# Performance work log

Measured on AMD Instinct MI355X. Metric: run time of the kernel, lower is better.

Reference implementation:

```python
import jax, jax.numpy as jnp
import numpy as np

N_NODES = 20000
N_EDGES = 160000
F_IN = 512
HIDDEN = 512
N_CLASSES = 40


def setup_inputs() -> dict:
    key = jax.random.key(0)
    k1, k2, k3, k4 = jax.random.split(key, 4)
    x = jax.random.normal(k1, (N_NODES, F_IN), dtype=jnp.float32)
    edge_index = jax.random.randint(k2, (2, N_EDGES), 0, N_NODES, dtype=jnp.int64)
    # Glorot-ish init scale for the linear weights
    W1 = jax.random.normal(k3, (F_IN, HIDDEN), dtype=jnp.float32) / np.sqrt(F_IN)
    b1 = jnp.zeros((HIDDEN,), dtype=jnp.float32)
    W2 = jax.random.normal(k4, (HIDDEN, N_CLASSES), dtype=jnp.float32) / np.sqrt(HIDDEN)
    b2 = jnp.zeros((N_CLASSES,), dtype=jnp.float32)
    return {"x": x, "edge_index": edge_index, "W1": W1, "b1": b1, "W2": W2, "b2": b2}


def _gcn_conv(x, W, b, src, dst, n_nodes):
    """PyG GCNConv: h = D^-1/2 (A+I) D^-1/2 (x W) + b, self-loops already in src/dst."""
    h = x @ W  # [N, out]
    deg = jax.ops.segment_sum(jnp.ones_like(dst, dtype=h.dtype), dst, num_segments=n_nodes)
    deg_inv_sqrt = jnp.where(deg > 0, jax.lax.rsqrt(jnp.maximum(deg, 1.0)), 0.0)
    norm = deg_inv_sqrt[src] * deg_inv_sqrt[dst]  # [E]
    msg = h[src] * norm[:, None]  # [E, out]
    return jax.ops.segment_sum(msg, dst, num_segments=n_nodes) + b


def reference(x, edge_index, W1, b1, W2, b2):
    n = x.shape[0]
    loop = jnp.arange(n, dtype=edge_index.dtype)
    src = jnp.concatenate([edge_index[0], loop])  # add self-loops
    dst = jnp.concatenate([edge_index[1], loop])
    h = _gcn_conv(x, W1, b1, src, dst, n)
    h = jax.nn.relu(h)
    # dropout(p=0.5) is identity in eval mode
    out = _gcn_conv(h, W2, b2, src, dst, n)
    return out
```

## Files before the change

kernel.cpp:

```cpp
#include <hip/hip_runtime.h>
#include <hip/hip_bf16.h>
#include <stdint.h>

#define N_NODES  20000
#define N_EDGES  160000
#define N_CLS    40
#define M_PAD    20096
#define CNT_PAD  20480
#define CAP      64

typedef __bf16 bf16;
typedef __attribute__((ext_vector_type(8))) __bf16 bf16x8;
typedef __attribute__((ext_vector_type(4))) float floatx4;

__device__ inline floatx4 zero4() { floatx4 z = {0.f, 0.f, 0.f, 0.f}; return z; }

typedef __attribute__((address_space(3))) uint32_t lds_u32;
typedef __attribute__((address_space(1))) const uint32_t glb_u32;
__device__ inline void ldst16(const void* g, void* l) {
    __builtin_amdgcn_global_load_lds((glb_u32*)g, (lds_u32*)l, 16, 0, 0);
}

struct Params {
    const float* x; const int* ei; const float* W1; const float* b1;
    const float* W2; const float* b2; float* out;
    bf16 *w1t, *w2p, *h1; float* h2;
    int *cnt, *colb;
};

#define S0_ZERO 20
#define S0_W1T  128
#define S0_W2P  96
#define S0_TOT  (S0_ZERO + S0_W1T + S0_W2P)
#define NB_G1   640
#define NB_FILL 625

__global__ __launch_bounds__(256) void k_s0(Params p) {
    const int vb = blockIdx.x, tid = threadIdx.x;
    if (vb < S0_ZERO) {
        int4* dz = (int4*)(p.cnt) + vb * 256 + tid;
        *dz = make_int4(0, 0, 0, 0);
    } else if (vb < S0_ZERO + S0_W1T) {
        int t  = (vb - S0_ZERO) * 256 + tid;
        int n  = t & 511;
        int k0 = (t >> 9) * 8;
        bf16x8 v;
        for (int j = 0; j < 8; ++j) v[j] = (bf16)p.W1[((k0 + j) << 9) + n];
        *(bf16x8*)(p.w1t + n * 512 + k0) = v;
    } else {
        int t = (vb - S0_ZERO - S0_W1T) * 256 + tid;
        int j = t & 7; int e = t >> 3;
        int lane = e & 63; e >>= 6;
        int nb = e % 3; int kt = e / 3;
        int k = kt * 32 + (lane >> 4) * 8 + j;
        int n = nb * 16 + (lane & 15);
        float v = (n < N_CLS) ? p.W2[k * N_CLS + n] : 0.f;
        p.w2p[t] = (bf16)v;
    }
}

__global__ __launch_bounds__(256) void k_g1f(Params p) {
    if (blockIdx.x >= NB_G1) {
        int e = (blockIdx.x - NB_G1) * 256 + threadIdx.x;
        if (e < N_EDGES) {
            int d = p.ei[N_EDGES + e];
            int j = atomicAdd(&p.cnt[d], 1);
            if (j < CAP) p.colb[d * CAP + j] = p.ei[e];
        }
        return;
    }
    const int g  = blockIdx.x;
    const int mi = (g >> 5) * 8 + (g & 7);
    const int ni = (g >> 3) & 3;
    if (mi >= 157) return;
    __shared__ float Asf[2][128 * 32];
    __shared__ bf16  Bs[2][128 * 32];
    const int tid  = threadIdx.x;
    const int lane = tid & 63;
    const int w    = tid >> 6;
    const int wm   = w >> 1, wn = w & 1;
    const int m0   = mi * 128;
    const int n0   = ni * 128;
    const int fr   = lane & 15, fq = lane >> 4;

    floatx4 acc[4][4];
    for (int mb = 0; mb < 4; ++mb)
        for (int nb = 0; nb < 4; ++nb) acc[mb][nb] = zero4();

    const int sr  = lane >> 2;
    const int skB = (((lane & 3) ^ ((lane >> 3) & 3))) * 8;
    const bf16* Bg = p.w1t + (long)(n0 + w * 32 + sr) * 512 + skB;

    const int arl = lane >> 3;
    const int ac  = (lane & 7) ^ arl;
    const float* Agp[4];
    for (int q = 0; q < 4; ++q) {
        int gr = m0 + w * 32 + q * 8 + arl;
        if (gr > N_NODES - 1) gr = N_NODES - 1;
        Agp[q] = p.x + (long)gr * 512 + ac * 4;
    }
    const int wofA = w * 1024;
    const int wofB = w * 1024;

    for (int q = 0; q < 4; ++q)
        ldst16(Agp[q], Asf[0] + wofA + q * 256);
    ldst16(Bg,            Bs[0] + wofB);
    ldst16(Bg + 16 * 512, Bs[0] + wofB + 512);

    const int fqsB = (fq ^ ((fr >> 1) & 3)) * 8;
    const int sA0  = (((fq << 1)    ) ^ (fr & 7)) * 4;
    const int sA1  = (((fq << 1) | 1) ^ (fr & 7)) * 4;

    for (int kt = 0; kt < 16; ++kt) {
        const int cur = kt & 1, nxt = cur ^ 1;
        __syncthreads();
        if (kt < 15) {
            const int k1 = (kt + 1) * 32;
            for (int q = 0; q < 4; ++q)
                ldst16(Agp[q] + k1, Asf[nxt] + wofA + q * 256);
            ldst16(Bg + k1,            Bs[nxt] + wofB);
            ldst16(Bg + k1 + 16 * 512, Bs[nxt] + wofB + 512);
        }
        bf16x8 af[4], bfv[4];
        for (int mb = 0; mb < 4; ++mb) {
            const float* rp = Asf[cur] + (wm * 64 + mb * 16 + fr) * 32;
            float4 lo = *(const float4*)(rp + sA0);
            float4 hi = *(const float4*)(rp + sA1);
            bf16x8 v;
            v[0] = (bf16)lo.x; v[1] = (bf16)lo.y; v[2] = (bf16)lo.z; v[3] = (bf16)lo.w;
            v[4] = (bf16)hi.x; v[5] = (bf16)hi.y; v[6] = (bf16)hi.z; v[7] = (bf16)hi.w;
            af[mb] = v;
        }
        for (int nb = 0; nb < 4; ++nb)
            bfv[nb] = *(const bf16x8*)(Bs[cur] + (wn * 64 + nb * 16 + fr) * 32 + fqsB);
        for (int mb = 0; mb < 4; ++mb)
            for (int nb = 0; nb < 4; ++nb)
                acc[mb][nb] = __builtin_amdgcn_mfma_f32_16x16x32_bf16(af[mb], bfv[nb], acc[mb][nb], 0, 0, 0);
    }
    for (int mb = 0; mb < 4; ++mb)
        for (int nb = 0; nb < 4; ++nb) {
            int row0 = m0 + wm * 64 + mb * 16 + fq * 4;
            int c    = n0 + wn * 64 + nb * 16 + fr;
            for (int r = 0; r < 4; ++r)
                p.h1[(long)(row0 + r) * 512 + c] = (bf16)acc[mb][nb][r];
        }
}

__global__ __launch_bounds__(256) void k_agg1g2(Params p) {
    __shared__ bf16 t[16 * 512];
    const int tid = threadIdx.x, l = tid & 63, w = tid >> 6;
    const int ib = blockIdx.x * 16;

    const float4* bp = (const float4*)(p.b1 + l * 8);
    float4 c0 = bp[0], c1 = bp[1];
    float bb[8] = {c0.x, c0.y, c0.z, c0.w, c1.x, c1.y, c1.z, c1.w};

    for (int q4 = 0; q4 < 4; ++q4) {
        const int r = w * 4 + q4;
        const int i = ib + r;
        bf16x8 o;
        if (i >= N_NODES) {
            for (int j = 0; j < 8; ++j) o[j] = (bf16)0.f;
        } else {
            const int ci = p.cnt[i];
            const float di = rsqrtf((float)(ci + 1));
            float acc[8];
            {
                bf16x8 v = *(const bf16x8*)(p.h1 + (long)i * 512 + l * 8);
                const float wi = di * di;
                for (int j = 0; j < 8; ++j) acc[j] = (float)v[j] * wi;
            }
            const int e1 = ci < CAP ? ci : CAP;
            const int* rowcol = p.colb + (long)i * CAP;
            int e = 0;
            for (; e + 8 <= e1; e += 8) {
                int4 sa = *(const int4*)(rowcol + e);
                int4 sb = *(const int4*)(rowcol + e + 4);
                float wgt[8];
                wgt[0] = rsqrtf((float)(p.cnt[sa.x] + 1)) * di;
                wgt[1] = rsqrtf((float)(p.cnt[sa.y] + 1)) * di;
                wgt[2] = rsqrtf((float)(p.cnt[sa.z] + 1)) * di;
                wgt[3] = rsqrtf((float)(p.cnt[sa.w] + 1)) * di;
                wgt[4] = rsqrtf((float)(p.cnt[sb.x] + 1)) * di;
                wgt[5] = rsqrtf((float)(p.cnt[sb.y] + 1)) * di;
                wgt[6] = rsqrtf((float)(p.cnt[sb.z] + 1)) * di;
                wgt[7] = rsqrtf((float)(p.cnt[sb.w] + 1)) * di;
                bf16x8 u[8];
                u[0] = *(const bf16x8*)(p.h1 + (long)sa.x * 512 + l * 8);
                u[1] = *(const bf16x8*)(p.h1 + (long)sa.y * 512 + l * 8);
                u[2] = *(const bf16x8*)(p.h1 + (long)sa.z * 512 + l * 8);
                u[3] = *(const bf16x8*)(p.h1 + (long)sa.w * 512 + l * 8);
                u[4] = *(const bf16x8*)(p.h1 + (long)sb.x * 512 + l * 8);
                u[5] = *(const bf16x8*)(p.h1 + (long)sb.y * 512 + l * 8);
                u[6] = *(const bf16x8*)(p.h1 + (long)sb.z * 512 + l * 8);
                u[7] = *(const bf16x8*)(p.h1 + (long)sb.w * 512 + l * 8);
                for (int q = 0; q < 8; ++q)
                    for (int j = 0; j < 8; ++j) acc[j] += (float)u[q][j] * wgt[q];
            }
            for (; e + 4 <= e1; e += 4) {
                int4 ss = *(const int4*)(rowcol + e);
                float w0 = rsqrtf((float)(p.cnt[ss.x] + 1)) * di;
                float w1 = rsqrtf((float)(p.cnt[ss.y] + 1)) * di;
                float w2 = rsqrtf((float)(p.cnt[ss.z] + 1)) * di;
                float w3 = rsqrtf((float)(p.cnt[ss.w] + 1)) * di;
                bf16x8 u0 = *(const bf16x8*)(p.h1 + (long)ss.x * 512 + l * 8);
                bf16x8 u1 = *(const bf16x8*)(p.h1 + (long)ss.y * 512 + l * 8);
                bf16x8 u2 = *(const bf16x8*)(p.h1 + (long)ss.z * 512 + l * 8);
                bf16x8 u3 = *(const bf16x8*)(p.h1 + (long)ss.w * 512 + l * 8);
                for (int j = 0; j < 8; ++j)
                    acc[j] += (float)u0[j] * w0 + (float)u1[j] * w1 + (float)u2[j] * w2 + (float)u3[j] * w3;
            }
            for (; e < e1; ++e) {
                int s = rowcol[e];
                float wt = rsqrtf((float)(p.cnt[s] + 1)) * di;
                bf16x8 u = *(const bf16x8*)(p.h1 + (long)s * 512 + l * 8);
                for (int j = 0; j < 8; ++j) acc[j] += (float)u[j] * wt;
            }
            for (int j = 0; j < 8; ++j) {
                float f = acc[j] + bb[j];
                f = f > 0.f ? f : 0.f;
                o[j] = (bf16)f;
            }
        }
        *(bf16x8*)((char*)t + r * 1024 + ((l * 16) ^ ((r & 7) << 4))) = o;
    }
    __syncthreads();
    if (w < 3) {
        const int fr = l & 15, fq = l >> 4;
        const int nb = w;
        floatx4 acc2 = zero4();
        for (int kt = 0; kt < 16; ++kt) {
            bf16x8 af = *(const bf16x8*)((const char*)t + fr * 1024 +
                                         ((kt * 64 + fq * 16) ^ ((fr & 7) << 4)));
            bf16x8 bfr = *(const bf16x8*)(p.w2p + ((kt * 3 + nb) * 64 + l) * 8);
            acc2 = __builtin_amdgcn_mfma_f32_16x16x32_bf16(af, bfr, acc2, 0, 0, 0);
        }
        for (int r2 = 0; r2 < 4; ++r2)
            p.h2[(long)(ib + fq * 4 + r2) * 48 + nb * 16 + fr] = acc2[r2];
    }
}

__global__ __launch_bounds__(256) void k_agg2(Params p) {
    const int i = blockIdx.x * 4 + (threadIdx.x >> 6);
    const int l = threadIdx.x & 63;
    if (i >= N_NODES || l >= N_CLS) return;
    const int ci = p.cnt[i];
    const float di = rsqrtf((float)(ci + 1));
    float acc = p.h2[(long)i * 48 + l] * di * di;
    const int e1 = ci < CAP ? ci : CAP;
    const int* rowcol = p.colb + (long)i * CAP;
    int e = 0;
    for (; e + 4 <= e1; e += 4) {
        int4 ss = *(const int4*)(rowcol + e);
        acc += p.h2[(long)ss.x * 48 + l] * (rsqrtf((float)(p.cnt[ss.x] + 1)) * di)
             + p.h2[(long)ss.y * 48 + l] * (rsqrtf((float)(p.cnt[ss.y] + 1)) * di)
             + p.h2[(long)ss.z * 48 + l] * (rsqrtf((float)(p.cnt[ss.z] + 1)) * di)
             + p.h2[(long)ss.w * 48 + l] * (rsqrtf((float)(p.cnt[ss.w] + 1)) * di);
    }
    for (; e < e1; ++e) {
        int s = rowcol[e];
        acc += p.h2[(long)s * 48 + l] * (rsqrtf((float)(p.cnt[s] + 1)) * di);
    }
    p.out[(long)i * N_CLS + l] = acc + p.b2[l];
}


extern "C" void kernel_launch(void* const* d_in, const int* in_sizes, int n_in,
                              void* d_out, int out_size, void* d_ws, size_t ws_size,
                              hipStream_t stream) {
    Params p;
    p.x  = (const float*)d_in[0];
    p.ei = (const int*)d_in[1];
    p.W1 = (const float*)d_in[2];
    p.b1 = (const float*)d_in[3];
    p.W2 = (const float*)d_in[4];
    p.b2 = (const float*)d_in[5];
    p.out = (float*)d_out;

    char* base = (char*)d_ws;
    size_t o = 0;
    auto alloc = [&](size_t bytes) { size_t r = o; o = (o + bytes + 255) & ~(size_t)255; return r; };
    p.w1t  = (bf16*)(base + alloc((size_t)512 * 512 * 2));
    p.w2p  = (bf16*)(base + alloc((size_t)24576 * 2));
    p.h1   = (bf16*)(base + alloc((size_t)M_PAD * 512 * 2));
    p.h2   = (float*)(base + alloc((size_t)M_PAD * 48 * 4));
    p.cnt  = (int*)(base + alloc((size_t)CNT_PAD * 4));
    p.colb = (int*)(base + alloc((size_t)N_NODES * CAP * 4));

    k_s0    <<<S0_TOT,           256, 0, stream>>>(p);
    k_g1f   <<<NB_G1 + NB_FILL,  256, 0, stream>>>(p);
    k_agg1g2<<<M_PAD / 16,       256, 0, stream>>>(p);
    k_agg2  <<<N_NODES / 4,      256, 0, stream>>>(p);
}
```

Measured before the change: 152.4 us.

## Widen first GEMM tile to 128x256 to halve A-tile conversions

The first-layer GEMM block tile grows from 128x128 to 128x256 in N. Grid blocks drop from 640 to 320 and each wave keeps a 4x8 accumulator array. The fp32 x tile is loaded and converted to bf16 half as many times overall, and each A fragment feeds twice as many MFMAs. The cost is about 128 accumulator registers per thread and more LDS per block. Launch bounds of 2 and fewer blocks may reduce occupancy and latency hiding.

```diff
diff --git a/kernel.cpp b/kernel.cpp
--- a/kernel.cpp
+++ b/kernel.cpp
@@ -32,7 +32,7 @@
 #define S0_W1T  128
 #define S0_W2P  96
 #define S0_TOT  (S0_ZERO + S0_W1T + S0_W2P)
-#define NB_G1   640
+#define NB_G1   320
 #define NB_FILL 625
 
 __global__ __launch_bounds__(256) void k_s0(Params p) {
@@ -59,7 +59,7 @@
     }
 }
 
-__global__ __launch_bounds__(256) void k_g1f(Params p) {
+__global__ __launch_bounds__(256, 2) void k_g1f(Params p) {
     if (blockIdx.x >= NB_G1) {
         int e = (blockIdx.x - NB_G1) * 256 + threadIdx.x;
         if (e < N_EDGES) {
@@ -70,42 +70,47 @@
         return;
     }
     const int g  = blockIdx.x;
-    const int mi = (g >> 5) * 8 + (g & 7);
-    const int ni = (g >> 3) & 3;
+    const int mi = (g >> 4) * 8 + (g & 7);
+    const int ni = (g >> 3) & 1;
     if (mi >= 157) return;
     __shared__ float Asf[2][128 * 32];
-    __shared__ bf16  Bs[2][128 * 32];
+    __shared__ bf16  Bs[2][256 * 32];
     const int tid  = threadIdx.x;
     const int lane = tid & 63;
     const int w    = tid >> 6;
     const int wm   = w >> 1, wn = w & 1;
     const int m0   = mi * 128;
-    const int n0   = ni * 128;
+    const int n0   = ni * 256;
     const int fr   = lane & 15, fq = lane >> 4;
 
-    floatx4 acc[4][4];
+    floatx4 acc[4][8];
+#pragma unroll
     for (int mb = 0; mb < 4; ++mb)
-        for (int nb = 0; nb < 4; ++nb) acc[mb][nb] = zero4();
+#pragma unroll
+        for (int nb = 0; nb < 8; ++nb) acc[mb][nb] = zero4();
 
     const int sr  = lane >> 2;
     const int skB = (((lane & 3) ^ ((lane >> 3) & 3))) * 8;
-    const bf16* Bg = p.w1t + (long)(n0 + w * 32 + sr) * 512 + skB;
+    const bf16* Bg = p.w1t + (long)(n0 + w * 64 + sr) * 512 + skB;
 
     const int arl = lane >> 3;
     const int ac  = (lane & 7) ^ arl;
     const float* Agp[4];
+#pragma unroll
     for (int q = 0; q < 4; ++q) {
         int gr = m0 + w * 32 + q * 8 + arl;
         if (gr > N_NODES - 1) gr = N_NODES - 1;
         Agp[q] = p.x + (long)gr * 512 + ac * 4;
     }
     const int wofA = w * 1024;
-    const int wofB = w * 1024;
-
+    const int wofB = w * 2048;
+
+#pragma unroll
     for (int q = 0; q < 4; ++q)
         ldst16(Agp[q], Asf[0] + wofA + q * 256);
-    ldst16(Bg,            Bs[0] + wofB);
-    ldst16(Bg + 16 * 512, Bs[0] + wofB + 512);
+#pragma unroll
+    for (int q = 0; q < 4; ++q)
+        ldst16(Bg + q * 16 * 512, Bs[0] + wofB + q * 512);
 
     const int fqsB = (fq ^ ((fr >> 1) & 3)) * 8;
     const int sA0  = (((fq << 1)    ) ^ (fr & 7)) * 4;
@@ -116,12 +121,15 @@
         __syncthreads();
         if (kt < 15) {
             const int k1 = (kt + 1) * 32;
+#pragma unroll
             for (int q = 0; q < 4; ++q)
                 ldst16(Agp[q] + k1, Asf[nxt] + wofA + q * 256);
-            ldst16(Bg + k1,            Bs[nxt] + wofB);
-            ldst16(Bg + k1 + 16 * 512, Bs[nxt] + wofB + 512);
-        }
-        bf16x8 af[4], bfv[4];
+#pragma unroll
+            for (int q = 0; q < 4; ++q)
+                ldst16(Bg + k1 + q * 16 * 512, Bs[nxt] + wofB + q * 512);
+        }
+        bf16x8 af[4];
+#pragma unroll
         for (int mb = 0; mb < 4; ++mb) {
             const float* rp = Asf[cur] + (wm * 64 + mb * 16 + fr) * 32;
             float4 lo = *(const float4*)(rp + sA0);
@@ -131,16 +139,21 @@
             v[4] = (bf16)hi.x; v[5] = (bf16)hi.y; v[6] = (bf16)hi.z; v[7] = (bf16)hi.w;
             af[mb] = v;
         }
-        for (int nb = 0; nb < 4; ++nb)
-            bfv[nb] = *(const bf16x8*)(Bs[cur] + (wn * 64 + nb * 16 + fr) * 32 + fqsB);
-        for (int mb = 0; mb < 4; ++mb)
-            for (int nb = 0; nb < 4; ++nb)
-                acc[mb][nb] = __builtin_amdgcn_mfma_f32_16x16x32_bf16(af[mb], bfv[nb], acc[mb][nb], 0, 0, 0);
-    }
+#pragma unroll
+        for (int nb = 0; nb < 8; ++nb) {
+            bf16x8 bv = *(const bf16x8*)(Bs[cur] + (wn * 128 + nb * 16 + fr) * 32 + fqsB);
+#pragma unroll
+            for (int mb = 0; mb < 4; ++mb)
+                acc[mb][nb] = __builtin_amdgcn_mfma_f32_16x16x32_bf16(af[mb], bv, acc[mb][nb], 0, 0, 0);
+        }
+    }
+#pragma unroll
     for (int mb = 0; mb < 4; ++mb)
-        for (int nb = 0; nb < 4; ++nb) {
+#pragma unroll
+        for (int nb = 0; nb < 8; ++nb) {
             int row0 = m0 + wm * 64 + mb * 16 + fq * 4;
-            int c    = n0 + wn * 64 + nb * 16 + fr;
+            int c    = n0 + wn * 128 + nb * 16 + fr;
+#pragma unroll
             for (int r = 0; r < 4; ++r)
                 p.h1[(long)(row0 + r) * 512 + c] = (bf16)acc[mb][nb][r];
         }
```

Result: slower. 160.7 us (+5.5%).
